# Performance work log

Measured on AMD Instinct MI355X. Metric: run time of the kernel, lower is better.

## Reference

```python
import jax, jax.numpy as jnp
import numpy as np

EMBED_DIM = 1024
NUM_HEADS = 16
HEAD_DIM = EMBED_DIM // NUM_HEADS
SCALING = HEAD_DIM ** -0.5
TGT, BSZ = 1024, 4


def setup_inputs() -> dict:
    key = jax.random.key(0)
    ks = jax.random.split(key, 8)
    query = jax.random.normal(ks[0], (TGT, BSZ, EMBED_DIM), dtype=jnp.float32)
    key_padding_mask = jax.random.randint(ks[1], (BSZ, TGT), 0, 2, dtype=jnp.int32)
    attn_mask = jax.random.normal(ks[2], (TGT, TGT), dtype=jnp.float32)
    attn_bias = jax.random.normal(ks[3], (BSZ * NUM_HEADS, TGT, TGT), dtype=jnp.float32)
    W_in = jax.random.normal(ks[4], (3 * EMBED_DIM, EMBED_DIM), dtype=jnp.float32) * 0.02
    b_in = jnp.zeros((3 * EMBED_DIM,), dtype=jnp.float32)
    W_out = jax.random.normal(ks[5], (EMBED_DIM, EMBED_DIM), dtype=jnp.float32) * 0.02
    b_out = jnp.zeros((EMBED_DIM,), dtype=jnp.float32)
    return {"query": query, "key_padding_mask": key_padding_mask,
            "attn_mask": attn_mask, "attn_bias": attn_bias,
            "W_in": W_in, "b_in": b_in, "W_out": W_out, "b_out": b_out}


def reference(query, key_padding_mask, attn_mask, attn_bias, W_in, b_in, W_out, b_out):
    tgt_len, bsz, embed_dim = query.shape
    # in_proj: (T,B,C) @ W_in.T -> (T,B,3C), chunk into q,k,v
    qkv = jnp.einsum('tbc,ec->tbe', query, W_in) + b_in
    q, k, v = jnp.split(qkv, 3, axis=-1)
    # reshape to (B*H, T, D)
    def to_bh(x):
        return x.reshape(tgt_len, bsz * NUM_HEADS, HEAD_DIM).transpose(1, 0, 2)
    q = to_bh(q) * SCALING
    k = to_bh(k)
    v = to_bh(v)
    src_len = k.shape[1]
    # scores: (B*H, T, S)
    attn_weights = jnp.einsum('ntd,nsd->nts', q, k)
    attn_weights = attn_weights + attn_mask[None, :, :]
    kpm = key_padding_mask.astype(bool)  # (B, S), True = pad
    aw = attn_weights.reshape(bsz, NUM_HEADS, tgt_len, src_len)
    aw = jnp.where(kpm[:, None, None, :], -jnp.inf, aw)
    attn_weights = aw.reshape(bsz * NUM_HEADS, tgt_len, src_len)
    attn_weights = attn_weights + attn_bias
    attn_probs = jax.nn.softmax(attn_weights, axis=-1)
    attn = jnp.einsum('nts,nsd->ntd', attn_probs, v)
    attn = attn.transpose(1, 0, 2).reshape(tgt_len, bsz, embed_dim)
    out = jnp.einsum('tbc,ec->tbe', attn, W_out) + b_out
    return out
```

## Files before the change

### kernel.cpp

```cpp
#include <hip/hip_runtime.h>

#define T_LEN 1024
#define B_SZ 4
#define EMB 1024
#define NH 16
#define HD 64

typedef _Float16 f16;
typedef __attribute__((ext_vector_type(8))) _Float16 f16x8;
typedef __attribute__((ext_vector_type(4))) _Float16 f16x4;
typedef __attribute__((ext_vector_type(4))) float f32x4;

__device__ __forceinline__ void gload16(const f16* g, f16* l) {
    __builtin_amdgcn_global_load_lds(
        (const __attribute__((address_space(1))) void*)g,
        (__attribute__((address_space(3))) void*)l, 16, 0, 0);
}

__global__ __launch_bounds__(256) void cvt_f32_to_f16(
    const float* __restrict__ in, f16* __restrict__ out, int n4)
{
    int i = blockIdx.x * 256 + threadIdx.x;
    if (i < n4) {
        float4 v = ((const float4*)in)[i];
        f16x4 h = { (f16)v.x, (f16)v.y, (f16)v.z, (f16)v.w };
        ((f16x4*)out)[i] = h;
    }
}

template<int MODE>
__global__ __launch_bounds__(256) void gemm_f16_v2(
    const f16* __restrict__ A, const f16* __restrict__ B,
    const float* __restrict__ bias, float* __restrict__ outF,
    f16* __restrict__ Qh, f16* __restrict__ Kh, f16* __restrict__ Vth,
    int M, int N, int K)
{
    __shared__ f16 As[128 * 32];
    __shared__ f16 Bs[128 * 32];
    const int tid = threadIdx.x;
    const int wv = tid >> 6, lane = tid & 63;
    const int lq = lane & 15, quad = lane >> 4;
    const int m0 = blockIdx.x * 128, n0 = blockIdx.y * 128;
    const int wm = (wv >> 1) * 64, wn = (wv & 1) * 64;

    const int s1 = tid, s2 = 256 + tid;
    const f16* a1 = A + (size_t)(m0 + (s1 >> 2)) * K + (s1 & 3) * 8;
    const f16* a2 = A + (size_t)(m0 + (s2 >> 2)) * K + (s2 & 3) * 8;
    const f16* b1 = B + (size_t)(n0 + (s1 >> 2)) * K + (s1 & 3) * 8;
    const f16* b2 = B + (size_t)(n0 + (s2 >> 2)) * K + (s2 & 3) * 8;
    f16* lA1 = As + s1 * 8; f16* lA2 = As + s2 * 8;
    f16* lB1 = Bs + s1 * 8; f16* lB2 = Bs + s2 * 8;

    f32x4 acc[4][4];
#pragma unroll
    for (int i = 0; i < 4; ++i)
#pragma unroll
        for (int j = 0; j < 4; ++j) acc[i][j] = (f32x4){0.f, 0.f, 0.f, 0.f};

    for (int k0 = 0; k0 < K; k0 += 32) {
        __syncthreads();
        gload16(a1 + k0, lA1);
        gload16(a2 + k0, lA2);
        gload16(b1 + k0, lB1);
        gload16(b2 + k0, lB2);
        __syncthreads();
        f16x8 af[4], bf[4];
#pragma unroll
        for (int t = 0; t < 4; ++t) {
            af[t] = *(const f16x8*)&As[(wm + t * 16 + lq) * 32 + quad * 8];
            bf[t] = *(const f16x8*)&Bs[(wn + t * 16 + lq) * 32 + quad * 8];
        }
#pragma unroll
        for (int mt = 0; mt < 4; ++mt)
#pragma unroll
            for (int nt = 0; nt < 4; ++nt)
                acc[mt][nt] = __builtin_amdgcn_mfma_f32_16x16x32_f16(
                    af[mt], bf[nt], acc[mt][nt], 0, 0, 0);
    }

#pragma unroll
    for (int nt = 0; nt < 4; ++nt) {
        const int col = n0 + wn + nt * 16 + lq;
        const float bb = bias[col];
        if (MODE == 0) {
#pragma unroll
            for (int mt = 0; mt < 4; ++mt)
#pragma unroll
                for (int r = 0; r < 4; ++r) {
                    const int row = m0 + wm + mt * 16 + quad * 4 + r;
                    outF[(size_t)row * N + col] = acc[mt][nt][r] + bb;
                }
        } else {
            const int sec = col >> 10, cc = col & 1023;
            const int h = cc >> 6, d = cc & 63;
#pragma unroll
            for (int mt = 0; mt < 4; ++mt)
#pragma unroll
                for (int r = 0; r < 4; ++r) {
                    const int row = m0 + wm + mt * 16 + quad * 4 + r;
                    const int t = row >> 2, b = row & 3;
                    const int bh = b * NH + h;
                    const f16 v = (f16)(acc[mt][nt][r] + bb);
                    if (sec == 0)      Qh[(size_t)bh * 65536 + t * 64 + d] = v;
                    else if (sec == 1) Kh[(size_t)bh * 65536 + t * 64 + d] = v;
                    else               Vth[(size_t)bh * 65536 + d * 1024 + t] = v;
                }
        }
    }
}

__global__ __launch_bounds__(256) void attn_v2(
    const f16* __restrict__ Qh, const f16* __restrict__ Kh,
    const f16* __restrict__ Vth, const int* __restrict__ kpm,
    const float* __restrict__ attn_mask, const float* __restrict__ attn_bias,
    f16* __restrict__ ctx)
{
    const int LDP = 72;
    __shared__ f16 Ps[4 * 16 * LDP];

    const int tid = threadIdx.x;
    const int wv = tid >> 6, lane = tid & 63;
    const int lq = lane & 15, quad = lane >> 4;
    const int q0 = blockIdx.x * 64;
    const int bh = blockIdx.y;
    const int b = bh >> 4, hh = bh & 15;

    const f16* Qb = Qh + (size_t)bh * 65536;
    const f16* Kb = Kh + (size_t)bh * 65536;
    const f16* Vb = Vth + (size_t)bh * 65536;
    f16* Pw = Ps + wv * 16 * LDP;

    const int t = q0 + wv * 16 + lq;
    const float* mrow = attn_mask + (size_t)t * T_LEN;
    const float* brow = attn_bias + ((size_t)bh * T_LEN + t) * T_LEN;
    const int* kpr = kpm + b * T_LEN;

    f16x8 bq[2];
    bq[0] = *(const f16x8*)(Qb + (size_t)t * 64 + quad * 8);
    bq[1] = *(const f16x8*)(Qb + (size_t)t * 64 + 32 + quad * 8);

    float m_i = -1e30f, l_i = 0.0f;
    f32x4 O[4];
#pragma unroll
    for (int dt = 0; dt < 4; ++dt) O[dt] = (f32x4){0.f, 0.f, 0.f, 0.f};

    for (int s0 = 0; s0 < T_LEN; s0 += 64) {
        f32x4 sacc[4];
#pragma unroll
        for (int st = 0; st < 4; ++st) sacc[st] = (f32x4){0.f, 0.f, 0.f, 0.f};
#pragma unroll
        for (int ks = 0; ks < 2; ++ks)
#pragma unroll
            for (int st = 0; st < 4; ++st) {
                const f16x8 ak = *(const f16x8*)(Kb + (size_t)(s0 + st * 16 + lq) * 64 + ks * 32 + quad * 8);
                sacc[st] = __builtin_amdgcn_mfma_f32_16x16x32_f16(ak, bq[ks], sacc[st], 0, 0, 0);
            }

        float4 m4[4], b4[4]; int4 kp4[4];
#pragma unroll
        for (int st = 0; st < 4; ++st) {
            const int sb = s0 + st * 16 + quad * 4;
            m4[st] = *(const float4*)(mrow + sb);
            b4[st] = *(const float4*)(brow + sb);
            kp4[st] = *(const int4*)(kpr + sb);
        }

        float sv[4][4];
        float rm = -1e30f;
#pragma unroll
        for (int st = 0; st < 4; ++st) {
            const float mv[4] = {m4[st].x, m4[st].y, m4[st].z, m4[st].w};
            const float bv[4] = {b4[st].x, b4[st].y, b4[st].z, b4[st].w};
            const int kv[4] = {kp4[st].x, kp4[st].y, kp4[st].z, kp4[st].w};
#pragma unroll
            for (int r = 0; r < 4; ++r) {
                const float x = sacc[st][r] * 0.125f + mv[r] + bv[r];
                sv[st][r] = kv[r] ? -1e30f : x;
                rm = fmaxf(rm, sv[st][r]);
            }
        }
        rm = fmaxf(rm, __shfl_xor(rm, 16));
        rm = fmaxf(rm, __shfl_xor(rm, 32));
        const float mn = fmaxf(m_i, rm);
        const float alpha = __expf(m_i - mn);
        m_i = mn;

        __builtin_amdgcn_wave_barrier();
        float rs = 0.0f;
#pragma unroll
        for (int st = 0; st < 4; ++st) {
            f16x4 pv;
#pragma unroll
            for (int r = 0; r < 4; ++r) {
                const float p = __expf(sv[st][r] - mn);
                rs += p;
                pv[r] = (f16)p;
            }
            *(f16x4*)&Pw[lq * LDP + st * 16 + quad * 4] = pv;
        }
        rs += __shfl_xor(rs, 16);
        rs += __shfl_xor(rs, 32);
        l_i = l_i * alpha + rs;

        float aB[4];
#pragma unroll
        for (int r = 0; r < 4; ++r) aB[r] = __shfl(alpha, quad * 4 + r, 16);
#pragma unroll
        for (int dt = 0; dt < 4; ++dt)
#pragma unroll
            for (int r = 0; r < 4; ++r) O[dt][r] *= aB[r];

        __builtin_amdgcn_wave_barrier();

#pragma unroll
        for (int ks = 0; ks < 2; ++ks) {
            const f16x8 ap = *(const f16x8*)&Pw[lq * LDP + ks * 32 + quad * 8];
#pragma unroll
            for (int dt = 0; dt < 4; ++dt) {
                const f16x8 av = *(const f16x8*)(Vb + (size_t)(dt * 16 + lq) * 1024 + s0 + ks * 32 + quad * 8);
                O[dt] = __builtin_amdgcn_mfma_f32_16x16x32_f16(ap, av, O[dt], 0, 0, 0);
            }
        }
    }

    float lB[4];
#pragma unroll
    for (int r = 0; r < 4; ++r) lB[r] = __shfl(l_i, quad * 4 + r, 16);
#pragma unroll
    for (int r = 0; r < 4; ++r) {
        const float inv = 1.0f / lB[r];
        const int tt = q0 + wv * 16 + quad * 4 + r;
#pragma unroll
        for (int dt = 0; dt < 4; ++dt)
            ctx[((size_t)tt * B_SZ + b) * EMB + hh * HD + dt * 16 + lq] = (f16)(O[dt][r] * inv);
    }
}

extern "C" void kernel_launch(void* const* d_in, const int* in_sizes, int n_in,
                              void* d_out, int out_size, void* d_ws, size_t ws_size,
                              hipStream_t stream)
{
    const float* query     = (const float*)d_in[0];
    const int*   kpm       = (const int*)  d_in[1];
    const float* attn_mask = (const float*)d_in[2];
    const float* attn_bias = (const float*)d_in[3];
    const float* W_in      = (const float*)d_in[4];
    const float* b_in      = (const float*)d_in[5];
    const float* W_out     = (const float*)d_in[6];
    const float* b_out     = (const float*)d_in[7];
    float* out = (float*)d_out;

    f16* q16    = (f16*)d_ws;
    f16* win16  = q16    + (size_t)4096 * 1024;
    f16* wout16 = win16  + (size_t)3072 * 1024;
    f16* Qh     = wout16 + (size_t)1024 * 1024;
    f16* Kh     = Qh     + (size_t)64 * 65536;
    f16* Vth    = Kh     + (size_t)64 * 65536;
    f16* ctx16  = Vth    + (size_t)64 * 65536;

    cvt_f32_to_f16<<<4096 * 1024 / 1024, 256, 0, stream>>>(query, q16,    4096 * 1024 / 4);
    cvt_f32_to_f16<<<3072 * 1024 / 1024, 256, 0, stream>>>(W_in,  win16,  3072 * 1024 / 4);
    cvt_f32_to_f16<<<1024 * 1024 / 1024, 256, 0, stream>>>(W_out, wout16, 1024 * 1024 / 4);

    dim3 g1(4096 / 128, 3072 / 128);
    gemm_f16_v2<2><<<g1, 256, 0, stream>>>(q16, win16, b_in, nullptr,
                                           Qh, Kh, Vth, 4096, 3072, 1024);

    dim3 g2(T_LEN / 64, B_SZ * NH);
    attn_v2<<<g2, 256, 0, stream>>>(Qh, Kh, Vth, kpm, attn_mask, attn_bias, ctx16);

    dim3 g3(4096 / 128, 1024 / 128);
    gemm_f16_v2<0><<<g3, 256, 0, stream>>>(ctx16, wout16, b_out, out,
                                           nullptr, nullptr, nullptr, 4096, 1024, 1024);
}
```

Baseline: 591.2 us.

## Swap GEMM operands for vectorized epilogue stores and prefetch attention operands

The GEMM kernel now treats weights as the M operand and activations as N. Each lane can then write four contiguous outputs with one vector store, replacing the scattered scalar stores of the old epilogue. The QKV projection writes a plain row-major qkv buffer, and a new LDS-tiled kernel transposes V into a per-head layout. Attention reads Q and K straight from the strided qkv buffer, prefetches K/V fragments before the MFMAs, and double-buffers the attention-bias loads one tile ahead. This adds an extra kernel launch and an extra pass over V, and K loads now stride 3072 elements per row, which may reduce coalescing.

```diff
diff --git a/kernel.cpp b/kernel.cpp
--- a/kernel.cpp
+++ b/kernel.cpp
@@ -5,6 +5,7 @@
 #define EMB 1024
 #define NH 16
 #define HD 64
+#define QKV_LD 3072
 
 typedef _Float16 f16;
 typedef __attribute__((ext_vector_type(8))) _Float16 f16x8;
@@ -28,12 +29,11 @@
     }
 }
 
-template<int MODE>
-__global__ __launch_bounds__(256) void gemm_f16_v2(
-    const f16* __restrict__ A, const f16* __restrict__ B,
-    const float* __restrict__ bias, float* __restrict__ outF,
-    f16* __restrict__ Qh, f16* __restrict__ Kh, f16* __restrict__ Vth,
-    int M, int N, int K)
+template<bool OUT_HALF>
+__global__ __launch_bounds__(256) void gemm_ct(
+    const f16* __restrict__ Wt, const f16* __restrict__ Xa,
+    const float* __restrict__ bias, void* __restrict__ Out,
+    int K, int ldo)
 {
     __shared__ f16 As[128 * 32];
     __shared__ f16 Bs[128 * 32];
@@ -44,10 +44,10 @@
     const int wm = (wv >> 1) * 64, wn = (wv & 1) * 64;
 
     const int s1 = tid, s2 = 256 + tid;
-    const f16* a1 = A + (size_t)(m0 + (s1 >> 2)) * K + (s1 & 3) * 8;
-    const f16* a2 = A + (size_t)(m0 + (s2 >> 2)) * K + (s2 & 3) * 8;
-    const f16* b1 = B + (size_t)(n0 + (s1 >> 2)) * K + (s1 & 3) * 8;
-    const f16* b2 = B + (size_t)(n0 + (s2 >> 2)) * K + (s2 & 3) * 8;
+    const f16* a1 = Wt + (size_t)(m0 + (s1 >> 2)) * K + (s1 & 3) * 8;
+    const f16* a2 = Wt + (size_t)(m0 + (s2 >> 2)) * K + (s2 & 3) * 8;
+    const f16* b1 = Xa + (size_t)(n0 + (s1 >> 2)) * K + (s1 & 3) * 8;
+    const f16* b2 = Xa + (size_t)(n0 + (s2 >> 2)) * K + (s2 & 3) * 8;
     f16* lA1 = As + s1 * 8; f16* lA2 = As + s2 * 8;
     f16* lB1 = Bs + s1 * 8; f16* lB2 = Bs + s2 * 8;
 
@@ -79,41 +79,57 @@
     }
 
 #pragma unroll
-    for (int nt = 0; nt < 4; ++nt) {
-        const int col = n0 + wn + nt * 16 + lq;
-        const float bb = bias[col];
-        if (MODE == 0) {
-#pragma unroll
-            for (int mt = 0; mt < 4; ++mt)
-#pragma unroll
-                for (int r = 0; r < 4; ++r) {
-                    const int row = m0 + wm + mt * 16 + quad * 4 + r;
-                    outF[(size_t)row * N + col] = acc[mt][nt][r] + bb;
-                }
-        } else {
-            const int sec = col >> 10, cc = col & 1023;
-            const int h = cc >> 6, d = cc & 63;
-#pragma unroll
-            for (int mt = 0; mt < 4; ++mt)
-#pragma unroll
-                for (int r = 0; r < 4; ++r) {
-                    const int row = m0 + wm + mt * 16 + quad * 4 + r;
-                    const int t = row >> 2, b = row & 3;
-                    const int bh = b * NH + h;
-                    const f16 v = (f16)(acc[mt][nt][r] + bb);
-                    if (sec == 0)      Qh[(size_t)bh * 65536 + t * 64 + d] = v;
-                    else if (sec == 1) Kh[(size_t)bh * 65536 + t * 64 + d] = v;
-                    else               Vth[(size_t)bh * 65536 + d * 1024 + t] = v;
-                }
-        }
-    }
-}
-
-__global__ __launch_bounds__(256) void attn_v2(
-    const f16* __restrict__ Qh, const f16* __restrict__ Kh,
-    const f16* __restrict__ Vth, const int* __restrict__ kpm,
-    const float* __restrict__ attn_mask, const float* __restrict__ attn_bias,
-    f16* __restrict__ ctx)
+    for (int mt = 0; mt < 4; ++mt) {
+        const int e0 = m0 + wm + mt * 16 + quad * 4;
+        const float4 bb = *(const float4*)(bias + e0);
+#pragma unroll
+        for (int nt = 0; nt < 4; ++nt) {
+            const int xr = n0 + wn + nt * 16 + lq;
+            if (OUT_HALF) {
+                f16x4 h = { (f16)(acc[mt][nt][0] + bb.x), (f16)(acc[mt][nt][1] + bb.y),
+                            (f16)(acc[mt][nt][2] + bb.z), (f16)(acc[mt][nt][3] + bb.w) };
+                *(f16x4*)((f16*)Out + (size_t)xr * ldo + e0) = h;
+            } else {
+                float4 o = { acc[mt][nt][0] + bb.x, acc[mt][nt][1] + bb.y,
+                             acc[mt][nt][2] + bb.z, acc[mt][nt][3] + bb.w };
+                *(float4*)((float*)Out + (size_t)xr * ldo + e0) = o;
+            }
+        }
+    }
+}
+
+__global__ __launch_bounds__(256) void vtrans(
+    const f16* __restrict__ qkv, f16* __restrict__ Vth)
+{
+    __shared__ f16 Ls[256 * 66];
+    const int bh = blockIdx.x;
+    const int t0 = blockIdx.y * 256;
+    const int b = bh >> 4, hh = bh & 15;
+    const int tid = threadIdx.x;
+
+#pragma unroll
+    for (int p = 0; p < 8; ++p) {
+        const int g = p * 2048 + tid * 8;
+        const int ti = g >> 6, dj = g & 63;
+        f16x8 v = *(const f16x8*)(qkv + (size_t)((t0 + ti) * 4 + b) * QKV_LD + 2048 + hh * 64 + dj);
+        *(f16x8*)&Ls[ti * 66 + dj] = v;
+    }
+    __syncthreads();
+#pragma unroll
+    for (int p = 0; p < 8; ++p) {
+        const int g = p * 2048 + tid * 8;
+        const int d = g >> 8, tt = g & 255;
+        f16x8 o;
+#pragma unroll
+        for (int j = 0; j < 8; ++j) o[j] = Ls[(tt + j) * 66 + d];
+        *(f16x8*)(Vth + (size_t)bh * 65536 + (size_t)d * 1024 + t0 + tt) = o;
+    }
+}
+
+__global__ __launch_bounds__(256) void attn_v3(
+    const f16* __restrict__ qkv, const f16* __restrict__ Vth,
+    const int* __restrict__ kpm, const float* __restrict__ attn_mask,
+    const float* __restrict__ attn_bias, f16* __restrict__ ctx)
 {
     const int LDP = 72;
     __shared__ f16 Ps[4 * 16 * LDP];
@@ -124,46 +140,70 @@
     const int q0 = blockIdx.x * 64;
     const int bh = blockIdx.y;
     const int b = bh >> 4, hh = bh & 15;
-
-    const f16* Qb = Qh + (size_t)bh * 65536;
-    const f16* Kb = Kh + (size_t)bh * 65536;
-    const f16* Vb = Vth + (size_t)bh * 65536;
     f16* Pw = Ps + wv * 16 * LDP;
 
     const int t = q0 + wv * 16 + lq;
     const float* mrow = attn_mask + (size_t)t * T_LEN;
     const float* brow = attn_bias + ((size_t)bh * T_LEN + t) * T_LEN;
     const int* kpr = kpm + b * T_LEN;
+    const f16* Vb = Vth + (size_t)bh * 65536;
 
     f16x8 bq[2];
-    bq[0] = *(const f16x8*)(Qb + (size_t)t * 64 + quad * 8);
-    bq[1] = *(const f16x8*)(Qb + (size_t)t * 64 + 32 + quad * 8);
+    {
+        const f16* qrow = qkv + (size_t)(t * 4 + b) * QKV_LD + hh * 64;
+        bq[0] = *(const f16x8*)(qrow + quad * 8);
+        bq[1] = *(const f16x8*)(qrow + 32 + quad * 8);
+    }
 
     float m_i = -1e30f, l_i = 0.0f;
     f32x4 O[4];
 #pragma unroll
     for (int dt = 0; dt < 4; ++dt) O[dt] = (f32x4){0.f, 0.f, 0.f, 0.f};
 
+    float4 b4[4];
+#pragma unroll
+    for (int st = 0; st < 4; ++st)
+        b4[st] = *(const float4*)(brow + st * 16 + quad * 4);
+
     for (int s0 = 0; s0 < T_LEN; s0 += 64) {
-        f32x4 sacc[4];
-#pragma unroll
-        for (int st = 0; st < 4; ++st) sacc[st] = (f32x4){0.f, 0.f, 0.f, 0.f};
+        f16x8 ak[2][4];
 #pragma unroll
         for (int ks = 0; ks < 2; ++ks)
 #pragma unroll
-            for (int st = 0; st < 4; ++st) {
-                const f16x8 ak = *(const f16x8*)(Kb + (size_t)(s0 + st * 16 + lq) * 64 + ks * 32 + quad * 8);
-                sacc[st] = __builtin_amdgcn_mfma_f32_16x16x32_f16(ak, bq[ks], sacc[st], 0, 0, 0);
-            }
-
-        float4 m4[4], b4[4]; int4 kp4[4];
+            for (int st = 0; st < 4; ++st)
+                ak[ks][st] = *(const f16x8*)(qkv
+                    + (size_t)((s0 + st * 16 + lq) * 4 + b) * QKV_LD
+                    + EMB + hh * 64 + ks * 32 + quad * 8);
+        f16x8 av[2][4];
+#pragma unroll
+        for (int ks = 0; ks < 2; ++ks)
+#pragma unroll
+            for (int dt = 0; dt < 4; ++dt)
+                av[ks][dt] = *(const f16x8*)(Vb + (size_t)(dt * 16 + lq) * 1024
+                                             + s0 + ks * 32 + quad * 8);
+        float4 m4[4]; int4 kp4[4];
 #pragma unroll
         for (int st = 0; st < 4; ++st) {
             const int sb = s0 + st * 16 + quad * 4;
             m4[st] = *(const float4*)(mrow + sb);
-            b4[st] = *(const float4*)(brow + sb);
             kp4[st] = *(const int4*)(kpr + sb);
         }
+        float4 b4n[4];
+        if (s0 + 64 < T_LEN) {
+#pragma unroll
+            for (int st = 0; st < 4; ++st)
+                b4n[st] = *(const float4*)(brow + s0 + 64 + st * 16 + quad * 4);
+        }
+
+        f32x4 sacc[4];
+#pragma unroll
+        for (int st = 0; st < 4; ++st) sacc[st] = (f32x4){0.f, 0.f, 0.f, 0.f};
+#pragma unroll
+        for (int ks = 0; ks < 2; ++ks)
+#pragma unroll
+            for (int st = 0; st < 4; ++st)
+                sacc[st] = __builtin_amdgcn_mfma_f32_16x16x32_f16(
+                    ak[ks][st], bq[ks], sacc[st], 0, 0, 0);
 
         float sv[4][4];
         float rm = -1e30f;
@@ -216,11 +256,13 @@
         for (int ks = 0; ks < 2; ++ks) {
             const f16x8 ap = *(const f16x8*)&Pw[lq * LDP + ks * 32 + quad * 8];
 #pragma unroll
-            for (int dt = 0; dt < 4; ++dt) {
-                const f16x8 av = *(const f16x8*)(Vb + (size_t)(dt * 16 + lq) * 1024 + s0 + ks * 32 + quad * 8);
-                O[dt] = __builtin_amdgcn_mfma_f32_16x16x32_f16(ap, av, O[dt], 0, 0, 0);
-            }
-        }
+            for (int dt = 0; dt < 4; ++dt)
+                O[dt] = __builtin_amdgcn_mfma_f32_16x16x32_f16(
+                    ap, av[ks][dt], O[dt], 0, 0, 0);
+        }
+
+#pragma unroll
+        for (int st = 0; st < 4; ++st) b4[st] = b4n[st];
     }
 
     float lB[4];
@@ -253,23 +295,23 @@
     f16* q16    = (f16*)d_ws;
     f16* win16  = q16    + (size_t)4096 * 1024;
     f16* wout16 = win16  + (size_t)3072 * 1024;
-    f16* Qh     = wout16 + (size_t)1024 * 1024;
-    f16* Kh     = Qh     + (size_t)64 * 65536;
-    f16* Vth    = Kh     + (size_t)64 * 65536;
+    f16* qkv16  = wout16 + (size_t)1024 * 1024;
+    f16* Vth    = qkv16  + (size_t)4096 * 3072;
     f16* ctx16  = Vth    + (size_t)64 * 65536;
 
     cvt_f32_to_f16<<<4096 * 1024 / 1024, 256, 0, stream>>>(query, q16,    4096 * 1024 / 4);
     cvt_f32_to_f16<<<3072 * 1024 / 1024, 256, 0, stream>>>(W_in,  win16,  3072 * 1024 / 4);
     cvt_f32_to_f16<<<1024 * 1024 / 1024, 256, 0, stream>>>(W_out, wout16, 1024 * 1024 / 4);
 
-    dim3 g1(4096 / 128, 3072 / 128);
-    gemm_f16_v2<2><<<g1, 256, 0, stream>>>(q16, win16, b_in, nullptr,
-                                           Qh, Kh, Vth, 4096, 3072, 1024);
+    dim3 g1(3072 / 128, 4096 / 128);
+    gemm_ct<true><<<g1, 256, 0, stream>>>(win16, q16, b_in, qkv16, 1024, QKV_LD);
+
+    dim3 gv(64, 4);
+    vtrans<<<gv, 256, 0, stream>>>(qkv16, Vth);
 
     dim3 g2(T_LEN / 64, B_SZ * NH);
-    attn_v2<<<g2, 256, 0, stream>>>(Qh, Kh, Vth, kpm, attn_mask, attn_bias, ctx16);
-
-    dim3 g3(4096 / 128, 1024 / 128);
-    gemm_f16_v2<0><<<g3, 256, 0, stream>>>(ctx16, wout16, b_out, out,
-                                           nullptr, nullptr, nullptr, 4096, 1024, 1024);
-}
+    attn_v3<<<g2, 256, 0, stream>>>(qkv16, Vth, kpm, attn_mask, attn_bias, ctx16);
+
+    dim3 g3(1024 / 128, 4096 / 128);
+    gemm_ct<false><<<g3, 256, 0, stream>>>(wout16, ctx16, b_out, out, 1024, 1024);
+}
```

Result: no change. 590.5 us (-0.1%).
